# Performance work log

Hardware: AMD Instinct MI355X
Metric: run time of the kernel (lower is better)

Reference implementation:

```python
import jax, jax.numpy as jnp
import numpy as np

N, E, D, H, C, ED = 30000, 300000, 256, 8, 32, 32
HID = H * C  # 256 = hidden_channels


def setup_inputs() -> dict:
    key = jax.random.key(0)
    ks = jax.random.split(key, 14)
    w = lambda k, shp, fan: (jax.random.normal(k, shp, jnp.float32) / np.sqrt(fan)).astype(jnp.float32)
    return {
        "x": jax.random.normal(ks[0], (N, D), jnp.float32),
        "edge_index": jax.random.randint(ks[1], (2, E), 0, N, jnp.int32),
        "edge_attr": jax.random.normal(ks[2], (E, ED), jnp.float32),
        # TransformerConv params (PyG: q/k/v Linears have bias; lin_edge & lin_skip bias=False)
        "Wq": w(ks[3], (D, HID), D), "bq": 0.01 * jax.random.normal(ks[4], (HID,), jnp.float32),
        "Wk": w(ks[5], (D, HID), D), "bk": 0.01 * jax.random.normal(ks[6], (HID,), jnp.float32),
        "Wv": w(ks[7], (D, HID), D), "bv": 0.01 * jax.random.normal(ks[8], (HID,), jnp.float32),
        "We": w(ks[9], (ED, HID), ED),
        "Wskip": w(ks[10], (D, HID), D),
        # MLP([HID, HID, HID], gelu-tanh, plain_last=False): two Linear+act layers
        "W1": w(ks[11], (HID, HID), HID), "b1": jnp.zeros((HID,), jnp.float32),
        "W2": w(ks[12], (HID, HID), HID), "b2": jnp.zeros((HID,), jnp.float32),
    }


def reference(x, edge_index, edge_attr, Wq, bq, Wk, bk, Wv, bv, We, Wskip, W1, b1, W2, b2):
    src, dst = edge_index[0], edge_index[1]  # message flows src -> dst
    q = (x @ Wq + bq).reshape(N, H, C)
    k = (x @ Wk + bk).reshape(N, H, C)
    v = (x @ Wv + bv).reshape(N, H, C)
    e = (edge_attr @ We).reshape(E, H, C)
    k_e = k[src] + e                               # [E,H,C]
    v_e = v[src] + e                               # [E,H,C]
    logits = jnp.einsum('ehc,ehc->eh', q[dst], k_e) / np.sqrt(C)  # [E,H]
    # segment softmax over incoming edges of each dst node
    m = jax.ops.segment_max(logits, dst, num_segments=N)          # [N,H]
    a = jnp.exp(logits - m[dst])
    denom = jax.ops.segment_sum(a, dst, num_segments=N)           # [N,H]
    alpha = a / (denom[dst] + 1e-16)                              # [E,H]
    agg = jax.ops.segment_sum(alpha[:, :, None] * v_e, dst, num_segments=N)  # [N,H,C]
    out = agg.reshape(N, HID) + x @ Wskip          # concat heads + root skip
    # residual MLP: x + gelu(gelu(x W1 + b1) W2 + b2)
    h = jax.nn.gelu(out @ W1 + b1, approximate=True)
    h = jax.nn.gelu(h @ W2 + b2, approximate=True)
    return out + h
```

## Files before the change

### kernel.cpp

```cpp
#include <hip/hip_runtime.h>

#define NN 30000
#define NE 300000
#define HIDDEN 256

typedef __attribute__((ext_vector_type(8))) __bf16 bf16x8;
typedef __attribute__((ext_vector_type(4))) __bf16 bf16x4;
typedef __attribute__((ext_vector_type(4))) float float4v;

__device__ inline __bf16 f2bf(float f) {
  unsigned u = __builtin_bit_cast(unsigned, f);
  u += 0x7fffu + ((u >> 16) & 1u);
  unsigned short s = (unsigned short)(u >> 16);
  return __builtin_bit_cast(__bf16, s);
}
__device__ inline float bf2f(__bf16 b) {
  unsigned short s = __builtin_bit_cast(unsigned short, b);
  unsigned u = ((unsigned)s) << 16;
  return __builtin_bit_cast(float, u);
}
__device__ inline float gelu_tanh(float x) {
  float x3 = x * x * x;
  return 0.5f * x * (1.0f + tanhf(0.79788456080286536f * (x + 0.044715f * x3)));
}

__global__ __launch_bounds__(256) void prep_kernel(
    const float* __restrict__ Wq, const float* __restrict__ Wk, const float* __restrict__ Wv,
    const float* __restrict__ Wsk, const float* __restrict__ W1, const float* __restrict__ W2,
    const float* __restrict__ We, const float* __restrict__ bq, const float* __restrict__ bk,
    const float* __restrict__ bv, const float* __restrict__ x,
    __bf16* __restrict__ WTall, __bf16* __restrict__ WT1, __bf16* __restrict__ WT2,
    float* __restrict__ ball, float* __restrict__ WeT, __bf16* __restrict__ xb) {
  const int b = blockIdx.x;
  const int tid = threadIdx.x;
  if (b < 1792) {
    const int region = b >> 8;
    const int idx = ((b & 255) << 8) | tid;
    const int k = idx & 255, n = idx >> 8;
    float v;
    if (region == 3) {
      const int h = n >> 5, d = n & 31;
      const float* wq = Wq + (size_t)k * 256 + h * 32;
      const float* we = We + (size_t)d * 256 + h * 32;
      float s = 0.f;
#pragma unroll
      for (int c = 0; c < 32; ++c) s += wq[c] * we[c];
      v = s;
    } else {
      const float* W = (region == 0) ? Wq : (region == 1) ? Wk : (region == 2) ? Wv
                     : (region == 4) ? Wsk : (region == 5) ? W1 : W2;
      v = W[(size_t)k * 256 + n];
    }
    const __bf16 bv16 = f2bf(v);
    if (region < 5) WTall[(size_t)region * 65536 + idx] = bv16;
    else if (region == 5) WT1[idx] = bv16;
    else WT2[idx] = bv16;
  } else if (b < 1797) {
    const int j = (b - 1792) * 256 + tid;
    if (j < 1280) {
      float v = 0.f;
      if (j < 256) v = bq[j];
      else if (j < 512) v = bk[j - 256];
      else if (j < 768) v = bv[j - 512];
      else if (j < 1024) {
        const int col = j - 768, h = col >> 5, d = col & 31;
        const float* bqh = bq + h * 32;
        const float* we = We + (size_t)d * 256 + h * 32;
        float s = 0.f;
#pragma unroll
        for (int c = 0; c < 32; ++c) s += bqh[c] * we[c];
        v = s;
      }
      ball[j] = v;
    }
  } else if (b < 1829) {
    const int idx = (b - 1797) * 256 + tid;
    const int ch = idx >> 5, d = idx & 31;
    WeT[idx] = We[(size_t)d * 256 + ch];
  } else {
    const int t = (b - 1829) * 256 + tid;
    if (t < NN * 256 / 8) {
      const float* p = x + (size_t)t * 8;
      float4v f0 = *(const float4v*)(p);
      float4v f1 = *(const float4v*)(p + 4);
      bf16x8 o;
#pragma unroll
      for (int j = 0; j < 4; ++j) { o[j] = f2bf(f0[j]); o[j + 4] = f2bf(f1[j]); }
      *(bf16x8*)(xb + (size_t)t * 8) = o;
    }
  }
}

__global__ void zero_int_kernel(int* __restrict__ p, int n) {
  int i = blockIdx.x * 256 + threadIdx.x;
  if (i < n) p[i] = 0;
}

__global__ void count_deg_kernel(const int* __restrict__ dst, int* __restrict__ deg, int E) {
  int e = blockIdx.x * 256 + threadIdx.x;
  if (e < E) atomicAdd(&deg[dst[e]], 1);
}

__global__ __launch_bounds__(1024) void scan_kernel(const int* __restrict__ deg,
                                                    int* __restrict__ offs, int n) {
  __shared__ int part[1024];
  const int tid = threadIdx.x;
  const int per = (n + 1023) / 1024;
  const int base = tid * per;
  int s = 0;
  for (int j = 0; j < per; ++j) {
    int i = base + j;
    if (i < n) s += deg[i];
  }
  part[tid] = s;
  __syncthreads();
  for (int st = 1; st < 1024; st <<= 1) {
    int t = (tid >= st) ? part[tid - st] : 0;
    __syncthreads();
    part[tid] += t;
    __syncthreads();
  }
  int run = (tid > 0) ? part[tid - 1] : 0;
  for (int j = 0; j < per; ++j) {
    int i = base + j;
    if (i < n) { offs[i] = run; run += deg[i]; }
  }
  if (tid == 1023) offs[n] = part[1023];
}

__global__ void scatter_kernel(const int* __restrict__ srcIn, const int* __restrict__ dstIn,
                               const int* __restrict__ offs, int* __restrict__ cursor,
                               int* __restrict__ srcs, int* __restrict__ eids, int E) {
  int e = blockIdx.x * 256 + threadIdx.x;
  if (e >= E) return;
  int d = dstIn[e];
  int p = atomicAdd(&cursor[d], 1);
  int o = offs[d] + p;
  srcs[o] = srcIn[e];
  eids[o] = e;
}

__global__ void gather_ea_kernel(const float* __restrict__ ea, const int* __restrict__ eids,
                                 __bf16* __restrict__ eaC, int E) {
  int t = blockIdx.x * 256 + threadIdx.x;
  if (t >= E * 4) return;
  int o = t >> 2, part = t & 3;
  int e = eids[o];
  const float* src = ea + (size_t)e * 32 + part * 8;
  float4v f0 = *(const float4v*)(src);
  float4v f1 = *(const float4v*)(src + 4);
  bf16x8 b;
#pragma unroll
  for (int j = 0; j < 4; ++j) { b[j] = f2bf(f0[j]); b[j + 4] = f2bf(f1[j]); }
  *(bf16x8*)(eaC + (size_t)o * 32 + part * 8) = b;
}

template <int GX, int EPI, int MODE>
__global__ __launch_bounds__(256) void gemm_k4(
    const __bf16* __restrict__ A, const __bf16* __restrict__ Wt,
    const float* __restrict__ bias,
    float* __restrict__ Yf, __bf16* __restrict__ Ybf,
    __bf16* __restrict__ QGp, __bf16* __restrict__ KVp,
    const float* __restrict__ resid, int M, int gyTiles) {
  __shared__ char smem[128 * 264 * 2];
  __bf16* Bs = (__bf16*)smem;
  const int bid = blockIdx.x;
  const int stripe = bid / (8 * GX);
  const int rem = bid % (8 * GX);
  const int y8 = rem % 8;
  const int xt = rem / 8;
  const int y = stripe * 8 + y8;
  if (y >= gyTiles) return;
  const int n0 = xt * 128;

  {
    const int t = threadIdx.x;
#pragma unroll
    for (int i = 0; i < 16; ++i) {
      int g = i * 256 + t;
      int row = g >> 5;
      int c16 = g & 31;
      bf16x8 v = *(const bf16x8*)(Wt + (size_t)(n0 + row) * 256 + c16 * 8);
      *(bf16x8*)(Bs + row * 264 + c16 * 8) = v;
    }
  }
  __syncthreads();

  const int lane = threadIdx.x & 63;
  const int w = threadIdx.x >> 6;
  const int r = lane & 15;
  const int q = lane >> 4;
  const int mw = y * 128 + w * 32;
  int ar0 = mw + r;      if (ar0 >= M) ar0 = M - 1;
  int ar1 = mw + 16 + r; if (ar1 >= M) ar1 = M - 1;
  const int kq = q * 8;

  float4v acc[2][8];
#pragma unroll
  for (int i = 0; i < 2; ++i)
#pragma unroll
    for (int t = 0; t < 8; ++t) acc[i][t] = (float4v){0.f, 0.f, 0.f, 0.f};

#pragma unroll
  for (int kk = 0; kk < 256; kk += 32) {
    const int ka = kk + kq;
    bf16x8 a0 = *(const bf16x8*)(A + (size_t)ar0 * 256 + ka);
    bf16x8 a1 = *(const bf16x8*)(A + (size_t)ar1 * 256 + ka);
    bf16x8 b[8];
#pragma unroll
    for (int t = 0; t < 8; ++t)
      b[t] = *(const bf16x8*)(Bs + (t * 16 + r) * 264 + ka);
#pragma unroll
    for (int t = 0; t < 8; ++t) {
      acc[0][t] = __builtin_amdgcn_mfma_f32_16x16x32_bf16(a0, b[t], acc[0][t], 0, 0, 0);
      acc[1][t] = __builtin_amdgcn_mfma_f32_16x16x32_bf16(a1, b[t], acc[1][t], 0, 0, 0);
    }
  }
  __syncthreads();

  float* cs = (float*)smem + w * 4224;
#pragma unroll
  for (int t = 0; t < 8; ++t) {
    const int col = n0 + t * 16 + r;
    const float bb = bias ? bias[col] : 0.0f;
#pragma unroll
    for (int i2 = 0; i2 < 2; ++i2)
#pragma unroll
      for (int ii = 0; ii < 4; ++ii) {
        float v = acc[i2][t][ii] + bb;
        if constexpr (EPI == 2 || EPI == 3) v = gelu_tanh(v);
        cs[(i2 * 16 + q * 4 + ii) * 132 + t * 16 + r] = v;
      }
  }

  constexpr int NSTR = GX * 128;
  const int p = n0 >> 8;
  const int cbase = n0 & 255;
  __bf16* dstI = (p == 0 || p == 3) ? QGp : KVp;
  const int moff = (p >= 2) ? 4 : 0;
#pragma unroll
  for (int i = 0; i < 16; ++i) {
    const int rl = i * 2 + (lane >> 5);
    const int row = mw + rl;
    const int c4 = (lane & 31) * 4;
    float4v v = *(const float4v*)(cs + rl * 132 + c4);
    if (row < M) {
      if constexpr (MODE == 1) {
        if (p == 4) {
          *(float4v*)(Yf + (size_t)row * 256 + cbase + c4) = v;
        } else {
          bf16x4 b4;
          b4[0] = f2bf(v[0]); b4[1] = f2bf(v[1]); b4[2] = f2bf(v[2]); b4[3] = f2bf(v[3]);
          const int c = cbase + c4;
          *(bf16x4*)(dstI + (size_t)row * 512 + 2 * c + moff) = b4;
        }
      } else if constexpr (EPI == 1) {
        *(float4v*)(Yf + (size_t)row * NSTR + n0 + c4) = v;
      } else if constexpr (EPI == 3) {
        float4v rr = *(const float4v*)(resid + (size_t)row * NSTR + n0 + c4);
        v[0] += rr[0]; v[1] += rr[1]; v[2] += rr[2]; v[3] += rr[3];
        *(float4v*)(Yf + (size_t)row * NSTR + n0 + c4) = v;
      } else {
        bf16x4 b4;
        b4[0] = f2bf(v[0]); b4[1] = f2bf(v[1]); b4[2] = f2bf(v[2]); b4[3] = f2bf(v[3]);
        *(bf16x4*)(Ybf + (size_t)row * NSTR + n0 + c4) = b4;
      }
    }
  }
}

__global__ __launch_bounds__(256) void attn_kernel(
    const __bf16* __restrict__ QG, const __bf16* __restrict__ KV,
    const __bf16* __restrict__ eaC,
    const int* __restrict__ offs, const int* __restrict__ srcs,
    float* __restrict__ OUT, __bf16* __restrict__ AE) {
  __shared__ float sdn[4][64];
  __shared__ float sav[4][64][4], sae[4][64][4];
  const int lane = threadIdx.x & 63;
  const int w = threadIdx.x >> 6;
  const int n = blockIdx.x;
  const int c0 = lane * 4;
  const int sub = lane & 7;

  const bf16x8 qg = *(const bf16x8*)(QG + (size_t)n * 512 + lane * 8);
  const float q0 = bf2f(qg[0]), q1 = bf2f(qg[1]), q2 = bf2f(qg[2]), q3 = bf2f(qg[3]);
  const float g0 = bf2f(qg[4]), g1 = bf2f(qg[5]), g2 = bf2f(qg[6]), g3 = bf2f(qg[7]);

  float denom = 0.f;
  float4v accv = {0.f, 0.f, 0.f, 0.f};
  float4v acce = {0.f, 0.f, 0.f, 0.f};
  const int beg = offs[n], end = offs[n + 1];
  for (int i = beg + w; i < end; i += 4) {
    const int sn = srcs[i];
    const bf16x8 kv = *(const bf16x8*)(KV + (size_t)sn * 512 + lane * 8);
    const bf16x4 e4 = *(const bf16x4*)(eaC + (size_t)i * 32 + sub * 4);
    const float e0 = bf2f(e4[0]), e1 = bf2f(e4[1]), e2 = bf2f(e4[2]), e3 = bf2f(e4[3]);
    float part = q0 * bf2f(kv[0]) + q1 * bf2f(kv[1]) + q2 * bf2f(kv[2]) + q3 * bf2f(kv[3])
               + g0 * e0 + g1 * e1 + g2 * e2 + g3 * e3;
    part += __shfl_xor(part, 1);
    part += __shfl_xor(part, 2);
    part += __shfl_xor(part, 4);
    const float wgt = __expf(part * 0.17677669529663687f);
    denom += wgt;
    accv[0] += wgt * bf2f(kv[4]);
    accv[1] += wgt * bf2f(kv[5]);
    accv[2] += wgt * bf2f(kv[6]);
    accv[3] += wgt * bf2f(kv[7]);
    acce[0] += wgt * e0;
    acce[1] += wgt * e1;
    acce[2] += wgt * e2;
    acce[3] += wgt * e3;
  }
  sdn[w][lane] = denom;
#pragma unroll
  for (int j = 0; j < 4; ++j) { sav[w][lane][j] = accv[j]; sae[w][lane][j] = acce[j]; }
  __syncthreads();
  if (w == 0) {
    float D = 0.f;
    float4v av = {0.f, 0.f, 0.f, 0.f};
    float4v ae = {0.f, 0.f, 0.f, 0.f};
#pragma unroll
    for (int ww = 0; ww < 4; ++ww) {
      D += sdn[ww][lane];
#pragma unroll
      for (int j = 0; j < 4; ++j) { av[j] += sav[ww][lane][j]; ae[j] += sae[ww][lane][j]; }
    }
    const float inv = 1.0f / (D + 1e-16f);
    float4v o = *(const float4v*)(OUT + (size_t)n * 256 + c0);
#pragma unroll
    for (int j = 0; j < 4; ++j) o[j] += av[j] * inv;
    *(float4v*)(OUT + (size_t)n * 256 + c0) = o;
    bf16x4 aeb;
    aeb[0] = f2bf(ae[0] * inv); aeb[1] = f2bf(ae[1] * inv);
    aeb[2] = f2bf(ae[2] * inv); aeb[3] = f2bf(ae[3] * inv);
    *(bf16x4*)(AE + (size_t)n * 256 + c0) = aeb;
  }
}

__global__ __launch_bounds__(256) void post_kernel(
    const __bf16* __restrict__ AE, const float* __restrict__ WeT,
    float* __restrict__ OUT, __bf16* __restrict__ OUTh) {
  const int lane = threadIdx.x & 63;
  const int wave = threadIdx.x >> 6;
  const int c0 = lane * 4;
  const int hg = lane >> 3;

  float4v w4[4][8];
#pragma unroll
  for (int j = 0; j < 4; ++j)
#pragma unroll
    for (int s = 0; s < 8; ++s)
      w4[j][s] = *(const float4v*)(WeT + (size_t)(c0 + j) * 32 + s * 4);

  const int nbase = blockIdx.x * 64;
  for (int it = 0; it < 16; ++it) {
    const int n = nbase + it * 4 + wave;
    if (n >= NN) return;
    const __bf16* aerow = AE + (size_t)n * HIDDEN + hg * 32;
    float aef[32];
#pragma unroll
    for (int t = 0; t < 4; ++t) {
      bf16x8 a8 = *(const bf16x8*)(aerow + t * 8);
#pragma unroll
      for (int j = 0; j < 8; ++j) aef[t * 8 + j] = bf2f(a8[j]);
    }
    float4v o = *(const float4v*)(OUT + (size_t)n * HIDDEN + c0);
#pragma unroll
    for (int j = 0; j < 4; ++j) {
      float s = 0.f;
#pragma unroll
      for (int g = 0; g < 8; ++g) {
        s += aef[g * 4 + 0] * w4[j][g][0] + aef[g * 4 + 1] * w4[j][g][1]
           + aef[g * 4 + 2] * w4[j][g][2] + aef[g * 4 + 3] * w4[j][g][3];
      }
      o[j] += s;
    }
    *(float4v*)(OUT + (size_t)n * HIDDEN + c0) = o;
    bf16x4 ob;
    ob[0] = f2bf(o[0]); ob[1] = f2bf(o[1]); ob[2] = f2bf(o[2]); ob[3] = f2bf(o[3]);
    *(bf16x4*)(OUTh + (size_t)n * HIDDEN + c0) = ob;
  }
}

extern "C" void kernel_launch(void* const* d_in, const int* in_sizes, int n_in,
                              void* d_out, int out_size, void* d_ws, size_t ws_size,
                              hipStream_t stream) {
  (void)in_sizes; (void)n_in; (void)out_size; (void)ws_size;
  const float* x   = (const float*)d_in[0];
  const int*   ei  = (const int*)d_in[1];
  const float* ea  = (const float*)d_in[2];
  const float* Wq  = (const float*)d_in[3];
  const float* bq  = (const float*)d_in[4];
  const float* Wk  = (const float*)d_in[5];
  const float* bk  = (const float*)d_in[6];
  const float* Wv  = (const float*)d_in[7];
  const float* bv  = (const float*)d_in[8];
  const float* We  = (const float*)d_in[9];
  const float* Wsk = (const float*)d_in[10];
  const float* W1  = (const float*)d_in[11];
  const float* b1  = (const float*)d_in[12];
  const float* W2  = (const float*)d_in[13];
  const float* b2  = (const float*)d_in[14];
  float* out = (float*)d_out;

  char* ws = (char*)d_ws;
  size_t off = 0;
  auto alloc = [&](size_t bytes) -> char* {
    off = (off + 255) & ~(size_t)255;
    char* p = ws + off;
    off += bytes;
    return p;
  };
  __bf16* QG   = (__bf16*)alloc((size_t)NN * 512 * 2);
  __bf16* KV   = (__bf16*)alloc((size_t)NN * 512 * 2);
  __bf16* xb   = (__bf16*)alloc((size_t)NN * 256 * 2);
  __bf16* AE   = (__bf16*)alloc((size_t)NN * 256 * 2);
  __bf16* OUTh = (__bf16*)alloc((size_t)NN * 256 * 2);
  __bf16* eaC  = (__bf16*)alloc((size_t)NE * 32 * 2);
  __bf16* WTall = (__bf16*)alloc((size_t)1280 * 256 * 2);
  __bf16* WT1  = (__bf16*)alloc(256 * 256 * 2);
  __bf16* WT2  = (__bf16*)alloc(256 * 256 * 2);
  float*  ball = (float*)alloc(1280 * 4);
  float*  WeT  = (float*)alloc(256 * 32 * 4);
  int* deg    = (int*)alloc((size_t)2 * NN * 4);
  int* cursor = deg + NN;
  int* offs   = (int*)alloc((size_t)(NN + 1) * 4);
  int* srcs   = (int*)alloc((size_t)NE * 4);
  int* eids   = (int*)alloc((size_t)NE * 4);
  __bf16* H1 = AE;

  const int* srcIn = ei;
  const int* dstIn = ei + NE;

  const int prepBlocks = 1829 + (NN * 256 / 8 + 255) / 256;
  prep_kernel<<<prepBlocks, 256, 0, stream>>>(Wq, Wk, Wv, Wsk, W1, W2, We, bq, bk, bv, x,
                                              WTall, WT1, WT2, ball, WeT, xb);

  zero_int_kernel<<<(2 * NN + 255) / 256, 256, 0, stream>>>(deg, 2 * NN);
  count_deg_kernel<<<(NE + 255) / 256, 256, 0, stream>>>(dstIn, deg, NE);
  scan_kernel<<<1, 1024, 0, stream>>>(deg, offs, NN);
  scatter_kernel<<<(NE + 255) / 256, 256, 0, stream>>>(srcIn, dstIn, offs, cursor, srcs, eids, NE);
  gather_ea_kernel<<<(NE * 4 + 255) / 256, 256, 0, stream>>>(ea, eids, eaC, NE);

  const int gy = (NN + 127) / 128;
  const int stripes = (gy + 7) / 8;
  gemm_k4<10, 0, 1><<<stripes * 80, 256, 0, stream>>>(
      xb, WTall, ball, out, nullptr, QG, KV, nullptr, NN, gy);

  attn_kernel<<<NN, 256, 0, stream>>>(QG, KV, eaC, offs, srcs, out, AE);

  post_kernel<<<(NN + 63) / 64, 256, 0, stream>>>(AE, WeT, out, OUTh);

  gemm_k4<2, 2, 0><<<stripes * 16, 256, 0, stream>>>(
      OUTh, WT1, b1, nullptr, H1, nullptr, nullptr, nullptr, NN, gy);
  gemm_k4<2, 3, 0><<<stripes * 16, 256, 0, stream>>>(
      H1, WT2, b2, out, nullptr, nullptr, nullptr, out, NN, gy);
}
```

Before: 403.6 us.

## Fuse post projection into attention, merge deg zeroing into prep, double GEMM M-tile

The edge-feature projection that post_kernel applied (aggregated edge attrs times We^T) now runs inside attn_kernel's epilogue, using shared memory to broadcast each head's 32 aggregated values. This removes a kernel launch and the round trip of the AE buffer through global memory. The degree-array zeroing moves into prep_kernel as extra blocks, dropping another launch. The QKV GEMM gets a DR template that gives each block 256 rows, reusing the staged weight tile across twice as many rows at the cost of more accumulator registers and fewer blocks.

```diff
diff --git a/kernel.cpp b/kernel.cpp
--- a/kernel.cpp
+++ b/kernel.cpp
@@ -30,7 +30,8 @@
     const float* __restrict__ We, const float* __restrict__ bq, const float* __restrict__ bk,
     const float* __restrict__ bv, const float* __restrict__ x,
     __bf16* __restrict__ WTall, __bf16* __restrict__ WT1, __bf16* __restrict__ WT2,
-    float* __restrict__ ball, float* __restrict__ WeT, __bf16* __restrict__ xb) {
+    float* __restrict__ ball, float* __restrict__ WeT, int* __restrict__ deg,
+    __bf16* __restrict__ xb) {
   const int b = blockIdx.x;
   const int tid = threadIdx.x;
   if (b < 1792) {
@@ -77,8 +78,11 @@
     const int idx = (b - 1797) * 256 + tid;
     const int ch = idx >> 5, d = idx & 31;
     WeT[idx] = We[(size_t)d * 256 + ch];
+  } else if (b < 2064) {
+    const int i = (b - 1829) * 256 + tid;
+    if (i < 2 * NN) deg[i] = 0;
   } else {
-    const int t = (b - 1829) * 256 + tid;
+    const int t = (b - 2064) * 256 + tid;
     if (t < NN * 256 / 8) {
       const float* p = x + (size_t)t * 8;
       float4v f0 = *(const float4v*)(p);
@@ -89,11 +93,6 @@
       *(bf16x8*)(xb + (size_t)t * 8) = o;
     }
   }
-}
-
-__global__ void zero_int_kernel(int* __restrict__ p, int n) {
-  int i = blockIdx.x * 256 + threadIdx.x;
-  if (i < n) p[i] = 0;
 }
 
 __global__ void count_deg_kernel(const int* __restrict__ dst, int* __restrict__ deg, int E) {
@@ -155,8 +154,8 @@
   *(bf16x8*)(eaC + (size_t)o * 32 + part * 8) = b;
 }
 
-template <int GX, int EPI, int MODE>
-__global__ __launch_bounds__(256) void gemm_k4(
+template <int GX, int EPI, int MODE, int DR>
+__global__ __launch_bounds__(256) void gemm_k5(
     const __bf16* __restrict__ A, const __bf16* __restrict__ Wt,
     const float* __restrict__ bias,
     float* __restrict__ Yf, __bf16* __restrict__ Ybf,
@@ -190,80 +189,89 @@
   const int w = threadIdx.x >> 6;
   const int r = lane & 15;
   const int q = lane >> 4;
-  const int mw = y * 128 + w * 32;
-  int ar0 = mw + r;      if (ar0 >= M) ar0 = M - 1;
-  int ar1 = mw + 16 + r; if (ar1 >= M) ar1 = M - 1;
+  const int mw = y * (128 * DR) + w * (32 * DR);
+  int ar[2 * DR];
+#pragma unroll
+  for (int i = 0; i < 2 * DR; ++i) {
+    ar[i] = mw + i * 16 + r;
+    if (ar[i] >= M) ar[i] = M - 1;
+  }
   const int kq = q * 8;
 
-  float4v acc[2][8];
-#pragma unroll
-  for (int i = 0; i < 2; ++i)
+  float4v acc[2 * DR][8];
+#pragma unroll
+  for (int i = 0; i < 2 * DR; ++i)
 #pragma unroll
     for (int t = 0; t < 8; ++t) acc[i][t] = (float4v){0.f, 0.f, 0.f, 0.f};
 
 #pragma unroll
   for (int kk = 0; kk < 256; kk += 32) {
     const int ka = kk + kq;
-    bf16x8 a0 = *(const bf16x8*)(A + (size_t)ar0 * 256 + ka);
-    bf16x8 a1 = *(const bf16x8*)(A + (size_t)ar1 * 256 + ka);
+    bf16x8 a[2 * DR];
+#pragma unroll
+    for (int i = 0; i < 2 * DR; ++i)
+      a[i] = *(const bf16x8*)(A + (size_t)ar[i] * 256 + ka);
     bf16x8 b[8];
 #pragma unroll
     for (int t = 0; t < 8; ++t)
       b[t] = *(const bf16x8*)(Bs + (t * 16 + r) * 264 + ka);
 #pragma unroll
-    for (int t = 0; t < 8; ++t) {
-      acc[0][t] = __builtin_amdgcn_mfma_f32_16x16x32_bf16(a0, b[t], acc[0][t], 0, 0, 0);
-      acc[1][t] = __builtin_amdgcn_mfma_f32_16x16x32_bf16(a1, b[t], acc[1][t], 0, 0, 0);
-    }
+    for (int t = 0; t < 8; ++t)
+#pragma unroll
+      for (int i = 0; i < 2 * DR; ++i)
+        acc[i][t] = __builtin_amdgcn_mfma_f32_16x16x32_bf16(a[i], b[t], acc[i][t], 0, 0, 0);
   }
   __syncthreads();
 
   float* cs = (float*)smem + w * 4224;
-#pragma unroll
-  for (int t = 0; t < 8; ++t) {
-    const int col = n0 + t * 16 + r;
-    const float bb = bias ? bias[col] : 0.0f;
-#pragma unroll
-    for (int i2 = 0; i2 < 2; ++i2)
-#pragma unroll
-      for (int ii = 0; ii < 4; ++ii) {
-        float v = acc[i2][t][ii] + bb;
-        if constexpr (EPI == 2 || EPI == 3) v = gelu_tanh(v);
-        cs[(i2 * 16 + q * 4 + ii) * 132 + t * 16 + r] = v;
-      }
-  }
-
   constexpr int NSTR = GX * 128;
   const int p = n0 >> 8;
   const int cbase = n0 & 255;
   __bf16* dstI = (p == 0 || p == 3) ? QGp : KVp;
   const int moff = (p >= 2) ? 4 : 0;
-#pragma unroll
-  for (int i = 0; i < 16; ++i) {
-    const int rl = i * 2 + (lane >> 5);
-    const int row = mw + rl;
-    const int c4 = (lane & 31) * 4;
-    float4v v = *(const float4v*)(cs + rl * 132 + c4);
-    if (row < M) {
-      if constexpr (MODE == 1) {
-        if (p == 4) {
-          *(float4v*)(Yf + (size_t)row * 256 + cbase + c4) = v;
+
+#pragma unroll
+  for (int h = 0; h < DR; ++h) {
+#pragma unroll
+    for (int t = 0; t < 8; ++t) {
+      const int col = n0 + t * 16 + r;
+      const float bb = bias ? bias[col] : 0.0f;
+#pragma unroll
+      for (int i2 = 0; i2 < 2; ++i2)
+#pragma unroll
+        for (int ii = 0; ii < 4; ++ii) {
+          float v = acc[h * 2 + i2][t][ii] + bb;
+          if constexpr (EPI == 2 || EPI == 3) v = gelu_tanh(v);
+          cs[(i2 * 16 + q * 4 + ii) * 132 + t * 16 + r] = v;
+        }
+    }
+#pragma unroll
+    for (int i = 0; i < 16; ++i) {
+      const int rl = i * 2 + (lane >> 5);
+      const int row = mw + h * 32 + rl;
+      const int c4 = (lane & 31) * 4;
+      float4v v = *(const float4v*)(cs + rl * 132 + c4);
+      if (row < M) {
+        if constexpr (MODE == 1) {
+          if (p == 4) {
+            *(float4v*)(Yf + (size_t)row * 256 + cbase + c4) = v;
+          } else {
+            bf16x4 b4;
+            b4[0] = f2bf(v[0]); b4[1] = f2bf(v[1]); b4[2] = f2bf(v[2]); b4[3] = f2bf(v[3]);
+            const int c = cbase + c4;
+            *(bf16x4*)(dstI + (size_t)row * 512 + 2 * c + moff) = b4;
+          }
+        } else if constexpr (EPI == 1) {
+          *(float4v*)(Yf + (size_t)row * NSTR + n0 + c4) = v;
+        } else if constexpr (EPI == 3) {
+          float4v rr = *(const float4v*)(resid + (size_t)row * NSTR + n0 + c4);
+          v[0] += rr[0]; v[1] += rr[1]; v[2] += rr[2]; v[3] += rr[3];
+          *(float4v*)(Yf + (size_t)row * NSTR + n0 + c4) = v;
         } else {
           bf16x4 b4;
           b4[0] = f2bf(v[0]); b4[1] = f2bf(v[1]); b4[2] = f2bf(v[2]); b4[3] = f2bf(v[3]);
-          const int c = cbase + c4;
-          *(bf16x4*)(dstI + (size_t)row * 512 + 2 * c + moff) = b4;
+          *(bf16x4*)(Ybf + (size_t)row * NSTR + n0 + c4) = b4;
         }
-      } else if constexpr (EPI == 1) {
-        *(float4v*)(Yf + (size_t)row * NSTR + n0 + c4) = v;
-      } else if constexpr (EPI == 3) {
-        float4v rr = *(const float4v*)(resid + (size_t)row * NSTR + n0 + c4);
-        v[0] += rr[0]; v[1] += rr[1]; v[2] += rr[2]; v[3] += rr[3];
-        *(float4v*)(Yf + (size_t)row * NSTR + n0 + c4) = v;
-      } else {
-        bf16x4 b4;
-        b4[0] = f2bf(v[0]); b4[1] = f2bf(v[1]); b4[2] = f2bf(v[2]); b4[3] = f2bf(v[3]);
-        *(bf16x4*)(Ybf + (size_t)row * NSTR + n0 + c4) = b4;
       }
     }
   }
@@ -271,9 +279,9 @@
 
 __global__ __launch_bounds__(256) void attn_kernel(
     const __bf16* __restrict__ QG, const __bf16* __restrict__ KV,
-    const __bf16* __restrict__ eaC,
+    const __bf16* __restrict__ eaC, const float* __restrict__ WeT,
     const int* __restrict__ offs, const int* __restrict__ srcs,
-    float* __restrict__ OUT, __bf16* __restrict__ AE) {
+    float* __restrict__ OUT, __bf16* __restrict__ OUTh) {
   __shared__ float sdn[4][64];
   __shared__ float sav[4][64][4], sae[4][64][4];
   const int lane = threadIdx.x & 63;
@@ -326,59 +334,31 @@
       for (int j = 0; j < 4; ++j) { av[j] += sav[ww][lane][j]; ae[j] += sae[ww][lane][j]; }
     }
     const float inv = 1.0f / (D + 1e-16f);
+#pragma unroll
+    for (int j = 0; j < 4; ++j) sae[0][lane][j] = ae[j] * inv;
+    float4v w4[4][8];
+#pragma unroll
+    for (int j = 0; j < 4; ++j)
+#pragma unroll
+      for (int s = 0; s < 8; ++s)
+        w4[j][s] = *(const float4v*)(WeT + (size_t)(c0 + j) * 32 + s * 4);
+    const int hb = lane & ~7;
+    float dotv[4] = {0.f, 0.f, 0.f, 0.f};
+#pragma unroll
+    for (int s = 0; s < 8; ++s) {
+      const float a0 = sae[0][hb + s][0], a1 = sae[0][hb + s][1];
+      const float a2 = sae[0][hb + s][2], a3 = sae[0][hb + s][3];
+#pragma unroll
+      for (int j = 0; j < 4; ++j)
+        dotv[j] += a0 * w4[j][s][0] + a1 * w4[j][s][1] + a2 * w4[j][s][2] + a3 * w4[j][s][3];
+    }
     float4v o = *(const float4v*)(OUT + (size_t)n * 256 + c0);
 #pragma unroll
-    for (int j = 0; j < 4; ++j) o[j] += av[j] * inv;
+    for (int j = 0; j < 4; ++j) o[j] += av[j] * inv + dotv[j];
     *(float4v*)(OUT + (size_t)n * 256 + c0) = o;
-    bf16x4 aeb;
-    aeb[0] = f2bf(ae[0] * inv); aeb[1] = f2bf(ae[1] * inv);
-    aeb[2] = f2bf(ae[2] * inv); aeb[3] = f2bf(ae[3] * inv);
-    *(bf16x4*)(AE + (size_t)n * 256 + c0) = aeb;
-  }
-}
-
-__global__ __launch_bounds__(256) void post_kernel(
-    const __bf16* __restrict__ AE, const float* __restrict__ WeT,
-    float* __restrict__ OUT, __bf16* __restrict__ OUTh) {
-  const int lane = threadIdx.x & 63;
-  const int wave = threadIdx.x >> 6;
-  const int c0 = lane * 4;
-  const int hg = lane >> 3;
-
-  float4v w4[4][8];
-#pragma unroll
-  for (int j = 0; j < 4; ++j)
-#pragma unroll
-    for (int s = 0; s < 8; ++s)
-      w4[j][s] = *(const float4v*)(WeT + (size_t)(c0 + j) * 32 + s * 4);
-
-  const int nbase = blockIdx.x * 64;
-  for (int it = 0; it < 16; ++it) {
-    const int n = nbase + it * 4 + wave;
-    if (n >= NN) return;
-    const __bf16* aerow = AE + (size_t)n * HIDDEN + hg * 32;
-    float aef[32];
-#pragma unroll
-    for (int t = 0; t < 4; ++t) {
-      bf16x8 a8 = *(const bf16x8*)(aerow + t * 8);
-#pragma unroll
-      for (int j = 0; j < 8; ++j) aef[t * 8 + j] = bf2f(a8[j]);
-    }
-    float4v o = *(const float4v*)(OUT + (size_t)n * HIDDEN + c0);
-#pragma unroll
-    for (int j = 0; j < 4; ++j) {
-      float s = 0.f;
-#pragma unroll
-      for (int g = 0; g < 8; ++g) {
-        s += aef[g * 4 + 0] * w4[j][g][0] + aef[g * 4 + 1] * w4[j][g][1]
-           + aef[g * 4 + 2] * w4[j][g][2] + aef[g * 4 + 3] * w4[j][g][3];
-      }
-      o[j] += s;
-    }
-    *(float4v*)(OUT + (size_t)n * HIDDEN + c0) = o;
     bf16x4 ob;
     ob[0] = f2bf(o[0]); ob[1] = f2bf(o[1]); ob[2] = f2bf(o[2]); ob[3] = f2bf(o[3]);
-    *(bf16x4*)(OUTh + (size_t)n * HIDDEN + c0) = ob;
+    *(bf16x4*)(OUTh + (size_t)n * 256 + c0) = ob;
   }
 }
 
@@ -414,8 +394,8 @@
   __bf16* QG   = (__bf16*)alloc((size_t)NN * 512 * 2);
   __bf16* KV   = (__bf16*)alloc((size_t)NN * 512 * 2);
   __bf16* xb   = (__bf16*)alloc((size_t)NN * 256 * 2);
-  __bf16* AE   = (__bf16*)alloc((size_t)NN * 256 * 2);
   __bf16* OUTh = (__bf16*)alloc((size_t)NN * 256 * 2);
+  __bf16* H1   = (__bf16*)alloc((size_t)NN * 256 * 2);
   __bf16* eaC  = (__bf16*)alloc((size_t)NE * 32 * 2);
   __bf16* WTall = (__bf16*)alloc((size_t)1280 * 256 * 2);
   __bf16* WT1  = (__bf16*)alloc(256 * 256 * 2);
@@ -427,32 +407,30 @@
   int* offs   = (int*)alloc((size_t)(NN + 1) * 4);
   int* srcs   = (int*)alloc((size_t)NE * 4);
   int* eids   = (int*)alloc((size_t)NE * 4);
-  __bf16* H1 = AE;
 
   const int* srcIn = ei;
   const int* dstIn = ei + NE;
 
-  const int prepBlocks = 1829 + (NN * 256 / 8 + 255) / 256;
+  const int prepBlocks = 2064 + (NN * 256 / 8 + 255) / 256;
   prep_kernel<<<prepBlocks, 256, 0, stream>>>(Wq, Wk, Wv, Wsk, W1, W2, We, bq, bk, bv, x,
-                                              WTall, WT1, WT2, ball, WeT, xb);
-
-  zero_int_kernel<<<(2 * NN + 255) / 256, 256, 0, stream>>>(deg, 2 * NN);
+                                              WTall, WT1, WT2, ball, WeT, deg, xb);
+
   count_deg_kernel<<<(NE + 255) / 256, 256, 0, stream>>>(dstIn, deg, NE);
   scan_kernel<<<1, 1024, 0, stream>>>(deg, offs, NN);
   scatter_kernel<<<(NE + 255) / 256, 256, 0, stream>>>(srcIn, dstIn, offs, cursor, srcs, eids, NE);
   gather_ea_kernel<<<(NE * 4 + 255) / 256, 256, 0, stream>>>(ea, eids, eaC, NE);
 
+  const int gy2 = (NN + 255) / 256;
+  const int stripes2 = (gy2 + 7) / 8;
+  gemm_k5<10, 0, 1, 2><<<stripes2 * 80, 256, 0, stream>>>(
+      xb, WTall, ball, out, nullptr, QG, KV, nullptr, NN, gy2);
+
+  attn_kernel<<<NN, 256, 0, stream>>>(QG, KV, eaC, WeT, offs, srcs, out, OUTh);
+
   const int gy = (NN + 127) / 128;
   const int stripes = (gy + 7) / 8;
-  gemm_k4<10, 0, 1><<<stripes * 80, 256, 0, stream>>>(
-      xb, WTall, ball, out, nullptr, QG, KV, nullptr, NN, gy);
-
-  attn_kernel<<<NN, 256, 0, stream>>>(QG, KV, eaC, offs, srcs, out, AE);
-
-  post_kernel<<<(NN + 63) / 64, 256, 0, stream>>>(AE, WeT, out, OUTh);
-
-  gemm_k4<2, 2, 0><<<stripes * 16, 256, 0, stream>>>(
+  gemm_k5<2, 2, 0, 1><<<stripes * 16, 256, 0, stream>>>(
       OUTh, WT1, b1, nullptr, H1, nullptr, nullptr, nullptr, NN, gy);
-  gemm_k4<2, 3, 0><<<stripes * 16, 256, 0, stream>>>(
+  gemm_k5<2, 3, 0, 1><<<stripes * 16, 256, 0, stream>>>(
       H1, WT2, b2, out, nullptr, nullptr, nullptr, out, NN, gy);
 }
```

Measured after the change: 506.9 us. 1.26x slower.
